# Optimization experiments

Hardware: AMD Instinct MI355X
Metric: run time of the kernel (lower is better)

## Reference

```python
import jax, jax.numpy as jnp
import numpy as np

B, P, C = 4, 2048, 1024
N_HEADS = 16
HEAD = C // N_HEADS


def setup_inputs() -> dict:
    key = jax.random.key(0)
    ks = jax.random.split(key, 9)
    s = C ** -0.5
    return {
        "x": jax.random.normal(ks[0], (B, P, C), dtype=jnp.float32),
        "Wq": jax.random.normal(ks[1], (C, C), dtype=jnp.float32) * s,
        "bq": jnp.zeros((C,), dtype=jnp.float32),
        "Wk": jax.random.normal(ks[2], (C, C), dtype=jnp.float32) * s,
        "bk": jnp.zeros((C,), dtype=jnp.float32),
        "Wv": jax.random.normal(ks[3], (C, C), dtype=jnp.float32) * s,
        "bv": jnp.zeros((C,), dtype=jnp.float32),
        "Wo": jax.random.normal(ks[4], (C, C), dtype=jnp.float32) * s,
        "bo": jnp.zeros((C,), dtype=jnp.float32),
    }


def _attn(x, Wq, bq, Wk, bk, Wv, bv, Wo, bo):
    b, p, c = x.shape
    q = (x @ Wq + bq).reshape(b, p, N_HEADS, HEAD).transpose(0, 2, 1, 3)
    k = (x @ Wk + bk).reshape(b, p, N_HEADS, HEAD).transpose(0, 2, 1, 3)
    v = (x @ Wv + bv).reshape(b, p, N_HEADS, HEAD).transpose(0, 2, 1, 3)
    # scores: [B, H, P, P]
    w = jnp.einsum('bhqd,bhkd->bhqk', q, k) * (HEAD ** -0.5)
    w = jax.nn.softmax(w, axis=-1)
    y = jnp.einsum('bhqk,bhkd->bhqd', w, v)
    y = y.transpose(0, 2, 1, 3).reshape(b, p, c)
    return y @ Wo + bo


def reference(x, Wq, bq, Wk, bk, Wv, bv, Wo, bo):
    return _attn(x, Wq, bq, Wk, bk, Wv, bv, Wo, bo)
```

## Files before the change

kernel.cpp:

```cpp
#include <hip/hip_runtime.h>

#define B_DIM 4
#define P_DIM 2048
#define C_DIM 1024
#define H_CNT 16
#define D_HEAD 64
#define M_DIM 8192
#define K_DIM 1024

typedef __attribute__((ext_vector_type(4))) float  f32x4;
typedef __attribute__((ext_vector_type(8))) __bf16 bf16x8;
typedef __attribute__((ext_vector_type(4))) short  s16x4;
typedef __attribute__((ext_vector_type(8))) short  s16x8;

static __device__ __forceinline__ short f2bf(float f) {
    unsigned u = __float_as_uint(f);
    u += 0x7fff + ((u >> 16) & 1);
    return (short)(u >> 16);
}

#define GLDS16(src, dst) __builtin_amdgcn_global_load_lds( \
    (__attribute__((address_space(1))) void*)(void*)(src), \
    (__attribute__((address_space(3))) void*)(void*)(dst), 16, 0, 0)

__global__ __launch_bounds__(256) void cvt_f32_bf16(const float* __restrict__ in,
                                                    short* __restrict__ out) {
    size_t i = ((size_t)blockIdx.x * 256 + threadIdx.x) * 4;
    f32x4 v = *(const f32x4*)(in + i);
    s16x4 o;
    o[0] = f2bf(v[0]); o[1] = f2bf(v[1]); o[2] = f2bf(v[2]); o[3] = f2bf(v[3]);
    *(s16x4*)(out + i) = o;
}

__global__ __launch_bounds__(256) void wtrans(const float* __restrict__ W,
                                              short* __restrict__ WT) {
    __shared__ float t[32][33];
    const int k0 = blockIdx.y * 32, n0 = blockIdx.x * 32;
    const int tx = threadIdx.x & 31, ty = threadIdx.x >> 5;
#pragma unroll
    for (int j = 0; j < 4; ++j)
        t[ty + j * 8][tx] = W[(size_t)(k0 + ty + j * 8) * C_DIM + n0 + tx];
    __syncthreads();
#pragma unroll
    for (int j = 0; j < 4; ++j)
        WT[(size_t)(n0 + ty + j * 8) * C_DIM + k0 + tx] = f2bf(t[tx][ty + j * 8]);
}

__global__ __launch_bounds__(256) void transpose_v(const short* __restrict__ v,
                                                   short* __restrict__ vt) {
    __shared__ short t[64][72];
    const int bh = blockIdx.y;
    const int p0 = blockIdx.x * 64;
    const short* src = v + ((size_t)bh * P_DIM + p0) * D_HEAD;
    short* dst = vt + (size_t)bh * D_HEAD * P_DIM + p0;
    const int tid = threadIdx.x;
#pragma unroll
    for (int s = 0; s < 2; ++s) {
        int row = (tid >> 3) + s * 32, ch = tid & 7;
        *(s16x8*)&t[row][ch * 8] = *(const s16x8*)&src[(size_t)row * D_HEAD + ch * 8];
    }
    __syncthreads();
#pragma unroll
    for (int s = 0; s < 2; ++s) {
        int d = (tid >> 3) + s * 32, ch = tid & 7;
        s16x8 val;
#pragma unroll
        for (int u = 0; u < 8; ++u) val[u] = t[ch * 8 + u][d];
        *(s16x8*)&dst[(size_t)d * P_DIM + ch * 8] = val;
    }
}

template<int MODE>
__global__ __launch_bounds__(256) void gemm_bt(const short* __restrict__ A,
                                               const short* __restrict__ BT,
                                               const float* __restrict__ bias,
                                               void* __restrict__ outp,
                                               float scale) {
    __shared__ __align__(16) short lA[128 * 32];
    __shared__ __align__(16) short lB[128 * 32];
    const int tid = threadIdx.x;
    const int lane = tid & 63;
    const int w = tid >> 6;
    const int m0 = blockIdx.y * 128;
    const int n0 = blockIdx.x * 128;
    const int wr = (w >> 1) * 64;
    const int wc = (w & 1) * 64;
    const int li = lane & 15, g = lane >> 4;

    f32x4 acc[4][4] = {};

    const int r0s = tid >> 2, r1s = (tid + 256) >> 2;
    const int c0 = (tid & 3) ^ ((r0s >> 1) & 3);
    const int c1 = (tid & 3) ^ ((r1s >> 1) & 3);
    const short* a0 = A + (size_t)(m0 + r0s) * K_DIM + c0 * 8;
    const short* a1 = A + (size_t)(m0 + r1s) * K_DIM + c1 * 8;
    const short* b0 = BT + (size_t)(n0 + r0s) * K_DIM + c0 * 8;
    const short* b1 = BT + (size_t)(n0 + r1s) * K_DIM + c1 * 8;
    short* lA0 = lA + w * 512;  short* lA1 = lA + 2048 + w * 512;
    short* lB0 = lB + w * 512;  short* lB1 = lB + 2048 + w * 512;

    int aoff[4], boff[4];
#pragma unroll
    for (int i = 0; i < 4; ++i) {
        int ra = wr + i * 16 + li;  int pa = g ^ ((ra >> 1) & 3);
        aoff[i] = ra * 32 + pa * 8;
        int rb = wc + i * 16 + li;  int pb = g ^ ((rb >> 1) & 3);
        boff[i] = rb * 32 + pb * 8;
    }

    for (int k0 = 0; k0 < K_DIM; k0 += 32) {
        __syncthreads();
        GLDS16(a0 + k0, lA0);
        GLDS16(a1 + k0, lA1);
        GLDS16(b0 + k0, lB0);
        GLDS16(b1 + k0, lB1);
        __syncthreads();
        bf16x8 af[4], bfr[4];
#pragma unroll
        for (int i = 0; i < 4; ++i) {
            af[i]  = *(const bf16x8*)&lA[aoff[i]];
            bfr[i] = *(const bf16x8*)&lB[boff[i]];
        }
#pragma unroll
        for (int i = 0; i < 4; ++i)
#pragma unroll
            for (int j = 0; j < 4; ++j)
                acc[i][j] = __builtin_amdgcn_mfma_f32_16x16x32_bf16(
                    af[i], bfr[j], acc[i][j], 0, 0, 0);
    }

#pragma unroll
    for (int j = 0; j < 4; ++j) {
        const int nn = n0 + wc + j * 16 + li;
        const float bb = bias[nn];
#pragma unroll
        for (int i = 0; i < 4; ++i) {
#pragma unroll
            for (int r = 0; r < 4; ++r) {
                const int mm = m0 + wr + i * 16 + 4 * g + r;
                float val = (acc[i][j][r] + bb) * scale;
                if (MODE == 0) {
                    int bI = mm >> 11, p = mm & 2047, hI = nn >> 6, d = nn & 63;
                    ((short*)outp)[(((size_t)bI * H_CNT + hI) * P_DIM + p) * D_HEAD + d] = f2bf(val);
                } else {
                    ((float*)outp)[(size_t)mm * C_DIM + nn] = val;
                }
            }
        }
    }
}

__global__ __launch_bounds__(256, 2) void attn_fwd(const short* __restrict__ Q,
                                                   const short* __restrict__ Kb,
                                                   const short* __restrict__ VT,
                                                   short* __restrict__ Y) {
    const int bh = blockIdx.y;
    const int b = bh >> 4, h = bh & 15;
    const int tid = threadIdx.x;
    const int w = tid >> 6, lane = tid & 63;
    const int li = lane & 15, g = lane >> 4;
    const int x7 = li & 7;
    const int q0 = blockIdx.x * 128 + w * 32;
    const short* Qh = Q + (size_t)bh * P_DIM * D_HEAD;
    const short* Kh = Kb + (size_t)bh * P_DIM * D_HEAD;
    const short* Vh = VT + (size_t)bh * D_HEAD * P_DIM;

    __shared__ __align__(16) short lK[64 * 64];
    __shared__ __align__(16) short lV[64 * 64];
    __shared__ __align__(16) short pb[4][32 * 64];
    short* pw = pb[w];

    bf16x8 qf[2][2];
#pragma unroll
    for (int qt = 0; qt < 2; ++qt)
#pragma unroll
        for (int c = 0; c < 2; ++c)
            qf[qt][c] = *(const bf16x8*)&Qh[(size_t)(q0 + qt * 16 + li) * D_HEAD + c * 32 + g * 8];

    f32x4 o[2][4] = {};
    f32x4 ps[2] = {};

    const int t1 = tid + 256;
    const int r0 = tid >> 3, u0 = (tid & 7) ^ (r0 & 7);
    const int r1 = t1 >> 3,  u1 = (t1 & 7) ^ (r1 & 7);
    const short* ks0 = Kh + r0 * D_HEAD + u0 * 8;
    const short* ks1 = Kh + r1 * D_HEAD + u1 * 8;
    const short* vs0 = Vh + r0 * P_DIM + u0 * 8;
    const short* vs1 = Vh + r1 * P_DIM + u1 * 8;
    short* dk0 = lK + tid * 8;  short* dk1 = lK + t1 * 8;
    short* dv0 = lV + tid * 8;  short* dv1 = lV + t1 * 8;

    for (int k0 = 0; k0 < P_DIM; k0 += 64) {
        __syncthreads();
        GLDS16(ks0 + (size_t)k0 * D_HEAD, dk0);
        GLDS16(ks1 + (size_t)k0 * D_HEAD, dk1);
        GLDS16(vs0 + k0, dv0);
        GLDS16(vs1 + k0, dv1);
        __syncthreads();

        f32x4 s[2][4] = {};
#pragma unroll
        for (int kt = 0; kt < 4; ++kt) {
            const int rbase = (kt * 16 + li) * 64;
            bf16x8 kf0 = *(const bf16x8*)&lK[rbase + ((0 + g) ^ x7) * 8];
            bf16x8 kf1 = *(const bf16x8*)&lK[rbase + ((4 + g) ^ x7) * 8];
#pragma unroll
            for (int qt = 0; qt < 2; ++qt) {
                s[qt][kt] = __builtin_amdgcn_mfma_f32_16x16x32_bf16(qf[qt][0], kf0, s[qt][kt], 0, 0, 0);
                s[qt][kt] = __builtin_amdgcn_mfma_f32_16x16x32_bf16(qf[qt][1], kf1, s[qt][kt], 0, 0, 0);
            }
        }
#pragma unroll
        for (int qt = 0; qt < 2; ++qt)
#pragma unroll
            for (int kt = 0; kt < 4; ++kt) {
                const int ub = kt * 2 + (li >> 3);
#pragma unroll
                for (int r = 0; r < 4; ++r) {
                    float e = __expf(s[qt][kt][r]);
                    ps[qt][r] += e;
                    const int row = qt * 16 + 4 * g + r;
                    *(__bf16*)&pw[row * 64 + (ub ^ (row & 7)) * 8 + x7] = (__bf16)e;
                }
            }
        __builtin_amdgcn_sched_barrier(0);
        asm volatile("s_waitcnt lgkmcnt(0)" ::: "memory");
        __builtin_amdgcn_sched_barrier(0);
#pragma unroll
        for (int kc = 0; kc < 2; ++kc) {
            bf16x8 pf[2];
#pragma unroll
            for (int qt = 0; qt < 2; ++qt) {
                const int row = qt * 16 + li;
                pf[qt] = *(const bf16x8*)&pw[row * 64 + ((kc * 4 + g) ^ x7) * 8];
            }
#pragma unroll
            for (int dt = 0; dt < 4; ++dt) {
                bf16x8 vf = *(const bf16x8*)&lV[(dt * 16 + li) * 64 + ((kc * 4 + g) ^ x7) * 8];
                o[0][dt] = __builtin_amdgcn_mfma_f32_16x16x32_bf16(pf[0], vf, o[0][dt], 0, 0, 0);
                o[1][dt] = __builtin_amdgcn_mfma_f32_16x16x32_bf16(pf[1], vf, o[1][dt], 0, 0, 0);
            }
        }
    }

#pragma unroll
    for (int qt = 0; qt < 2; ++qt)
#pragma unroll
        for (int r = 0; r < 4; ++r) {
            float v = ps[qt][r];
            v += __shfl_xor(v, 1);
            v += __shfl_xor(v, 2);
            v += __shfl_xor(v, 4);
            v += __shfl_xor(v, 8);
            ps[qt][r] = 1.0f / v;
        }
#pragma unroll
    for (int qt = 0; qt < 2; ++qt)
#pragma unroll
        for (int r = 0; r < 4; ++r) {
            const int p = q0 + qt * 16 + 4 * g + r;
            short* yrow = Y + ((size_t)b * P_DIM + p) * C_DIM + h * D_HEAD;
            const float inv = ps[qt][r];
#pragma unroll
            for (int dt = 0; dt < 4; ++dt)
                yrow[dt * 16 + li] = f2bf(o[qt][dt][r] * inv);
        }
}

extern "C" void kernel_launch(void* const* d_in, const int* in_sizes, int n_in,
                              void* d_out, int out_size, void* d_ws, size_t ws_size,
                              hipStream_t stream) {
    (void)in_sizes; (void)n_in; (void)out_size; (void)ws_size;
    const float* x  = (const float*)d_in[0];
    const float* Wq = (const float*)d_in[1];
    const float* bq = (const float*)d_in[2];
    const float* Wk = (const float*)d_in[3];
    const float* bk = (const float*)d_in[4];
    const float* Wv = (const float*)d_in[5];
    const float* bv = (const float*)d_in[6];
    const float* Wo = (const float*)d_in[7];
    const float* bo = (const float*)d_in[8];

    short* ws  = (short*)d_ws;
    short* xb  = ws;
    short* wqt = xb  + (size_t)M_DIM * C_DIM;
    short* wkt = wqt + (size_t)C_DIM * C_DIM;
    short* wvt = wkt + (size_t)C_DIM * C_DIM;
    short* wot = wvt + (size_t)C_DIM * C_DIM;
    short* qd  = wot + (size_t)C_DIM * C_DIM;
    short* kd  = qd  + (size_t)M_DIM * C_DIM;
    short* vd  = kd  + (size_t)M_DIM * C_DIM;
    short* vtd = vd  + (size_t)M_DIM * C_DIM;
    short* yd  = vtd + (size_t)M_DIM * C_DIM;

    cvt_f32_bf16<<<dim3(M_DIM * C_DIM / 1024), 256, 0, stream>>>(x, xb);
    wtrans<<<dim3(32, 32), 256, 0, stream>>>(Wq, wqt);
    wtrans<<<dim3(32, 32), 256, 0, stream>>>(Wk, wkt);
    wtrans<<<dim3(32, 32), 256, 0, stream>>>(Wv, wvt);
    wtrans<<<dim3(32, 32), 256, 0, stream>>>(Wo, wot);
    gemm_bt<0><<<dim3(8, 64), 256, 0, stream>>>(xb, wqt, bq, (void*)qd, 0.125f);
    gemm_bt<0><<<dim3(8, 64), 256, 0, stream>>>(xb, wkt, bk, (void*)kd, 1.0f);
    gemm_bt<0><<<dim3(8, 64), 256, 0, stream>>>(xb, wvt, bv, (void*)vd, 1.0f);
    transpose_v<<<dim3(32, 64), 256, 0, stream>>>(vd, vtd);
    attn_fwd<<<dim3(16, 64), 256, 0, stream>>>(qd, kd, vtd, yd);
    gemm_bt<1><<<dim3(8, 64), 256, 0, stream>>>(yd, wot, bo, d_out, 1.0f);
}
```

Baseline: 242.3 us.

## Double-buffer K/V tiles, enlarge attention query tile, fuse V transpose into GEMM

The attention kernel now gives each wave 64 query rows instead of 32, so each K/V tile loaded into LDS is reused across more queries. K/V tiles are double-buffered, with the next tile's loads issued before the current one is computed. The V projection GEMM writes its output already transposed, which removes the separate transpose kernel and its buffer. The log2(e) factor is folded into the Q scale so exp2f can replace __expf. The costs are more registers and more LDS per block, which may lower occupancy, and half as many attention blocks.

After: 250.2 us. 3.3% more time.

```diff
diff --git a/kernel.cpp b/kernel.cpp
--- a/kernel.cpp
+++ b/kernel.cpp
@@ -44,30 +44,6 @@
 #pragma unroll
     for (int j = 0; j < 4; ++j)
         WT[(size_t)(n0 + ty + j * 8) * C_DIM + k0 + tx] = f2bf(t[tx][ty + j * 8]);
-}
-
-__global__ __launch_bounds__(256) void transpose_v(const short* __restrict__ v,
-                                                   short* __restrict__ vt) {
-    __shared__ short t[64][72];
-    const int bh = blockIdx.y;
-    const int p0 = blockIdx.x * 64;
-    const short* src = v + ((size_t)bh * P_DIM + p0) * D_HEAD;
-    short* dst = vt + (size_t)bh * D_HEAD * P_DIM + p0;
-    const int tid = threadIdx.x;
-#pragma unroll
-    for (int s = 0; s < 2; ++s) {
-        int row = (tid >> 3) + s * 32, ch = tid & 7;
-        *(s16x8*)&t[row][ch * 8] = *(const s16x8*)&src[(size_t)row * D_HEAD + ch * 8];
-    }
-    __syncthreads();
-#pragma unroll
-    for (int s = 0; s < 2; ++s) {
-        int d = (tid >> 3) + s * 32, ch = tid & 7;
-        s16x8 val;
-#pragma unroll
-        for (int u = 0; u < 8; ++u) val[u] = t[ch * 8 + u][d];
-        *(s16x8*)&dst[(size_t)d * P_DIM + ch * 8] = val;
-    }
 }
 
 template<int MODE>
@@ -142,8 +118,11 @@
                 if (MODE == 0) {
                     int bI = mm >> 11, p = mm & 2047, hI = nn >> 6, d = nn & 63;
                     ((short*)outp)[(((size_t)bI * H_CNT + hI) * P_DIM + p) * D_HEAD + d] = f2bf(val);
+                } else if (MODE == 1) {
+                    ((float*)outp)[(size_t)mm * C_DIM + nn] = val;
                 } else {
-                    ((float*)outp)[(size_t)mm * C_DIM + nn] = val;
+                    int bI = mm >> 11, p = mm & 2047, hI = nn >> 6, d = nn & 63;
+                    ((short*)outp)[(((size_t)bI * H_CNT + hI) * D_HEAD + d) * P_DIM + p] = f2bf(val);
                 }
             }
         }
@@ -160,25 +139,25 @@
     const int w = tid >> 6, lane = tid & 63;
     const int li = lane & 15, g = lane >> 4;
     const int x7 = li & 7;
-    const int q0 = blockIdx.x * 128 + w * 32;
+    const int q0 = blockIdx.x * 256 + w * 64;
     const short* Qh = Q + (size_t)bh * P_DIM * D_HEAD;
     const short* Kh = Kb + (size_t)bh * P_DIM * D_HEAD;
     const short* Vh = VT + (size_t)bh * D_HEAD * P_DIM;
 
-    __shared__ __align__(16) short lK[64 * 64];
-    __shared__ __align__(16) short lV[64 * 64];
-    __shared__ __align__(16) short pb[4][32 * 64];
+    __shared__ __align__(16) short lK[2][64 * 64];
+    __shared__ __align__(16) short lV[2][64 * 64];
+    __shared__ __align__(16) short pb[4][64 * 64];
     short* pw = pb[w];
 
-    bf16x8 qf[2][2];
-#pragma unroll
-    for (int qt = 0; qt < 2; ++qt)
+    bf16x8 qf[4][2];
+#pragma unroll
+    for (int qt = 0; qt < 4; ++qt)
 #pragma unroll
         for (int c = 0; c < 2; ++c)
             qf[qt][c] = *(const bf16x8*)&Qh[(size_t)(q0 + qt * 16 + li) * D_HEAD + c * 32 + g * 8];
 
-    f32x4 o[2][4] = {};
-    f32x4 ps[2] = {};
+    f32x4 o[4][4] = {};
+    f32x4 ps[4] = {};
 
     const int t1 = tid + 256;
     const int r0 = tid >> 3, u0 = (tid & 7) ^ (r0 & 7);
@@ -187,64 +166,74 @@
     const short* ks1 = Kh + r1 * D_HEAD + u1 * 8;
     const short* vs0 = Vh + r0 * P_DIM + u0 * 8;
     const short* vs1 = Vh + r1 * P_DIM + u1 * 8;
-    short* dk0 = lK + tid * 8;  short* dk1 = lK + t1 * 8;
-    short* dv0 = lV + tid * 8;  short* dv1 = lV + t1 * 8;
-
-    for (int k0 = 0; k0 < P_DIM; k0 += 64) {
-        __syncthreads();
-        GLDS16(ks0 + (size_t)k0 * D_HEAD, dk0);
-        GLDS16(ks1 + (size_t)k0 * D_HEAD, dk1);
-        GLDS16(vs0 + k0, dv0);
-        GLDS16(vs1 + k0, dv1);
-        __syncthreads();
-
-        f32x4 s[2][4] = {};
+
+    GLDS16(ks0, &lK[0][tid * 8]);
+    GLDS16(ks1, &lK[0][t1 * 8]);
+    GLDS16(vs0, &lV[0][tid * 8]);
+    GLDS16(vs1, &lV[0][t1 * 8]);
+    __syncthreads();
+
+    for (int t = 0; t < P_DIM / 64; ++t) {
+        const int cur = t & 1;
+        if (t < P_DIM / 64 - 1) {
+            const int nk = (t + 1) * 64;
+            GLDS16(ks0 + (size_t)nk * D_HEAD, &lK[cur ^ 1][tid * 8]);
+            GLDS16(ks1 + (size_t)nk * D_HEAD, &lK[cur ^ 1][t1 * 8]);
+            GLDS16(vs0 + nk, &lV[cur ^ 1][tid * 8]);
+            GLDS16(vs1 + nk, &lV[cur ^ 1][t1 * 8]);
+        }
+        const short* K_ = lK[cur];
+        const short* V_ = lV[cur];
+
+        bf16x8 kf[4][2];
 #pragma unroll
         for (int kt = 0; kt < 4; ++kt) {
             const int rbase = (kt * 16 + li) * 64;
-            bf16x8 kf0 = *(const bf16x8*)&lK[rbase + ((0 + g) ^ x7) * 8];
-            bf16x8 kf1 = *(const bf16x8*)&lK[rbase + ((4 + g) ^ x7) * 8];
-#pragma unroll
-            for (int qt = 0; qt < 2; ++qt) {
-                s[qt][kt] = __builtin_amdgcn_mfma_f32_16x16x32_bf16(qf[qt][0], kf0, s[qt][kt], 0, 0, 0);
-                s[qt][kt] = __builtin_amdgcn_mfma_f32_16x16x32_bf16(qf[qt][1], kf1, s[qt][kt], 0, 0, 0);
-            }
-        }
-#pragma unroll
-        for (int qt = 0; qt < 2; ++qt)
+            kf[kt][0] = *(const bf16x8*)&K_[rbase + ((0 + g) ^ x7) * 8];
+            kf[kt][1] = *(const bf16x8*)&K_[rbase + ((4 + g) ^ x7) * 8];
+        }
+#pragma unroll
+        for (int qt = 0; qt < 4; ++qt) {
+            f32x4 s[4] = {};
+#pragma unroll
+            for (int kt = 0; kt < 4; ++kt) {
+                s[kt] = __builtin_amdgcn_mfma_f32_16x16x32_bf16(qf[qt][0], kf[kt][0], s[kt], 0, 0, 0);
+                s[kt] = __builtin_amdgcn_mfma_f32_16x16x32_bf16(qf[qt][1], kf[kt][1], s[kt], 0, 0, 0);
+            }
 #pragma unroll
             for (int kt = 0; kt < 4; ++kt) {
                 const int ub = kt * 2 + (li >> 3);
 #pragma unroll
                 for (int r = 0; r < 4; ++r) {
-                    float e = __expf(s[qt][kt][r]);
+                    float e = exp2f(s[kt][r]);
                     ps[qt][r] += e;
                     const int row = qt * 16 + 4 * g + r;
                     *(__bf16*)&pw[row * 64 + (ub ^ (row & 7)) * 8 + x7] = (__bf16)e;
                 }
             }
+        }
         __builtin_amdgcn_sched_barrier(0);
         asm volatile("s_waitcnt lgkmcnt(0)" ::: "memory");
         __builtin_amdgcn_sched_barrier(0);
 #pragma unroll
         for (int kc = 0; kc < 2; ++kc) {
-            bf16x8 pf[2];
-#pragma unroll
-            for (int qt = 0; qt < 2; ++qt) {
-                const int row = qt * 16 + li;
-                pf[qt] = *(const bf16x8*)&pw[row * 64 + ((kc * 4 + g) ^ x7) * 8];
-            }
-#pragma unroll
-            for (int dt = 0; dt < 4; ++dt) {
-                bf16x8 vf = *(const bf16x8*)&lV[(dt * 16 + li) * 64 + ((kc * 4 + g) ^ x7) * 8];
-                o[0][dt] = __builtin_amdgcn_mfma_f32_16x16x32_bf16(pf[0], vf, o[0][dt], 0, 0, 0);
-                o[1][dt] = __builtin_amdgcn_mfma_f32_16x16x32_bf16(pf[1], vf, o[1][dt], 0, 0, 0);
-            }
-        }
-    }
-
-#pragma unroll
-    for (int qt = 0; qt < 2; ++qt)
+            bf16x8 vf[4];
+#pragma unroll
+            for (int dt = 0; dt < 4; ++dt)
+                vf[dt] = *(const bf16x8*)&V_[(dt * 16 + li) * 64 + ((kc * 4 + g) ^ x7) * 8];
+#pragma unroll
+            for (int qt = 0; qt < 4; ++qt) {
+                bf16x8 pf = *(const bf16x8*)&pw[(qt * 16 + li) * 64 + ((kc * 4 + g) ^ x7) * 8];
+#pragma unroll
+                for (int dt = 0; dt < 4; ++dt)
+                    o[qt][dt] = __builtin_amdgcn_mfma_f32_16x16x32_bf16(pf, vf[dt], o[qt][dt], 0, 0, 0);
+            }
+        }
+        __syncthreads();
+    }
+
+#pragma unroll
+    for (int qt = 0; qt < 4; ++qt)
 #pragma unroll
         for (int r = 0; r < 4; ++r) {
             float v = ps[qt][r];
@@ -255,7 +244,7 @@
             ps[qt][r] = 1.0f / v;
         }
 #pragma unroll
-    for (int qt = 0; qt < 2; ++qt)
+    for (int qt = 0; qt < 4; ++qt)
 #pragma unroll
         for (int r = 0; r < 4; ++r) {
             const int p = q0 + qt * 16 + 4 * g + r;
@@ -289,8 +278,7 @@
     short* wot = wvt + (size_t)C_DIM * C_DIM;
     short* qd  = wot + (size_t)C_DIM * C_DIM;
     short* kd  = qd  + (size_t)M_DIM * C_DIM;
-    short* vd  = kd  + (size_t)M_DIM * C_DIM;
-    short* vtd = vd  + (size_t)M_DIM * C_DIM;
+    short* vtd = kd  + (size_t)M_DIM * C_DIM;
     short* yd  = vtd + (size_t)M_DIM * C_DIM;
 
     cvt_f32_bf16<<<dim3(M_DIM * C_DIM / 1024), 256, 0, stream>>>(x, xb);
@@ -298,10 +286,9 @@
     wtrans<<<dim3(32, 32), 256, 0, stream>>>(Wk, wkt);
     wtrans<<<dim3(32, 32), 256, 0, stream>>>(Wv, wvt);
     wtrans<<<dim3(32, 32), 256, 0, stream>>>(Wo, wot);
-    gemm_bt<0><<<dim3(8, 64), 256, 0, stream>>>(xb, wqt, bq, (void*)qd, 0.125f);
+    gemm_bt<0><<<dim3(8, 64), 256, 0, stream>>>(xb, wqt, bq, (void*)qd, 0.18033688011112042f);
     gemm_bt<0><<<dim3(8, 64), 256, 0, stream>>>(xb, wkt, bk, (void*)kd, 1.0f);
-    gemm_bt<0><<<dim3(8, 64), 256, 0, stream>>>(xb, wvt, bv, (void*)vd, 1.0f);
-    transpose_v<<<dim3(32, 64), 256, 0, stream>>>(vd, vtd);
-    attn_fwd<<<dim3(16, 64), 256, 0, stream>>>(qd, kd, vtd, yd);
+    gemm_bt<2><<<dim3(8, 64), 256, 0, stream>>>(xb, wvt, bv, (void*)vtd, 1.0f);
+    attn_fwd<<<dim3(8, 64), 256, 0, stream>>>(qd, kd, vtd, yd);
     gemm_bt<1><<<dim3(8, 64), 256, 0, stream>>>(yd, wot, bo, d_out, 1.0f);
 }
```
